# Performance work log

Hardware: AMD Instinct MI355X
Metric: run time of the kernel (lower is better)

Reference implementation:

```python
import jax, jax.numpy as jnp
import numpy as np

B, T, C = 8, 1024, 2048
N_HEAD = 16
HEAD = C // N_HEAD  # 128


def setup_inputs() -> dict:
    key = jax.random.key(0)
    k1, k2, k3 = jax.random.split(key, 3)
    scale = 0.02
    x = jax.random.normal(k1, (B, T, C), dtype=jnp.float32)
    W_attn = jax.random.normal(k2, (C, 3 * C), dtype=jnp.float32) * scale
    b_attn = jnp.zeros((3 * C,), dtype=jnp.float32)
    W_proj = jax.random.normal(k3, (C, C), dtype=jnp.float32) * scale
    b_proj = jnp.zeros((C,), dtype=jnp.float32)
    return {"x": x, "W_attn": W_attn, "b_attn": b_attn, "W_proj": W_proj, "b_proj": b_proj}


def reference(x, W_attn, b_attn, W_proj, b_proj):
    Bq, Tq, Cq = x.shape
    qkv = x @ W_attn + b_attn                       # [B,T,3C]
    q, k, v = jnp.split(qkv, 3, axis=2)             # each [B,T,C]
    def heads(t):
        return t.reshape(Bq, Tq, N_HEAD, HEAD).transpose(0, 2, 1, 3)  # [B,H,T,D]
    q, k, v = heads(q), heads(k), heads(v)
    scores = jnp.einsum('bhqd,bhkd->bhqk', q, k) / jnp.sqrt(jnp.float32(HEAD))
    causal = jnp.tril(jnp.ones((Tq, Tq), dtype=bool))
    scores = jnp.where(causal, scores, jnp.float32(-1e9))
    attn = jax.nn.softmax(scores, axis=-1)          # [B,H,T,T]
    y = jnp.einsum('bhqk,bhkd->bhqd', attn, v)      # [B,H,T,D]
    y = y.transpose(0, 2, 1, 3).reshape(Bq, Tq, Cq) # [B,T,C]
    return y @ W_proj + b_proj
```

## Files before the change

kernel.cpp:

```cpp
#include <hip/hip_runtime.h>
#include <hip/hip_bf16.h>


typedef unsigned short u16;
typedef __bf16 bf16x8 __attribute__((ext_vector_type(8)));
typedef float f32x4 __attribute__((ext_vector_type(4)));

#define B_ 8
#define T_ 1024
#define C_ 2048
#define NH 16
#define HD 128
#define BH (B_*NH)

__device__ __forceinline__ u16 f2b(float f){
  __bf16 h = (__bf16)f; return __builtin_bit_cast(u16, h);
}
__device__ __forceinline__ unsigned pk2(float x, float y){
  return (unsigned)f2b(x) | ((unsigned)f2b(y) << 16);
}
__device__ __forceinline__ bf16x8 ldfrag(const u16* p){
  uint4 u = *(const uint4*)p; return __builtin_bit_cast(bf16x8, u);
}
__device__ __forceinline__ void glds16(const u16* g, const u16* l){
  __builtin_amdgcn_global_load_lds(
      (const __attribute__((address_space(1))) void*)g,
      (__attribute__((address_space(3))) void*)l, 16, 0, 0);
}

__global__ __launch_bounds__(256) void cvt_bf16(
    const float4* __restrict__ in, ushort4* __restrict__ outp, int n4)
{
  int i = blockIdx.x*256 + threadIdx.x;
  const int stride = gridDim.x*256;
  for (; i < n4; i += stride){
    float4 f = in[i];
    ushort4 o; o.x = f2b(f.x); o.y = f2b(f.y); o.z = f2b(f.z); o.w = f2b(f.w);
    outp[i] = o;
  }
}

__global__ __launch_bounds__(256) void transpose_cvt(
    const float* __restrict__ in, u16* __restrict__ outp, int R, int C)
{
  __shared__ u16 tile[64][65];
  const int t = threadIdx.x;
  const int r0 = blockIdx.y * 64, c0 = blockIdx.x * 64;
#pragma unroll
  for (int ii = 0; ii < 16; ++ii){
    int idx = t + ii*256; int r = idx >> 6, c = idx & 63;
    tile[r][c] = f2b(in[(size_t)(r0 + r)*C + c0 + c]);
  }
  __syncthreads();
#pragma unroll
  for (int ii = 0; ii < 16; ++ii){
    int idx = t + ii*256; int r = idx >> 6, c = idx & 63;
    outp[(size_t)(c0 + r)*R + r0 + c] = tile[c][r];
  }
}

__device__ __forceinline__ void qkv_epilogue(
    const f32x4 acc[4][4], const float* bias, int bx, int by,
    int wm, int wn, int lq, int ln,
    u16* qb, u16* kb, u16* vb)
{
  const int tensor = bx >> 4, h = bx & 15, b = by >> 3, t0 = (by & 7)*128;
  u16* tb = tensor==0 ? qb : (tensor==1 ? kb : vb);
  u16* op = tb + ((size_t)(b*NH + h)*T_ + t0)*HD;
#pragma unroll
  for (int j=0;j<4;j++){
    const float bv = bias[bx*128 + wn*64 + j*16 + ln];
    const int n = wn*64 + j*16 + ln;
#pragma unroll
    for (int i=0;i<4;i++){
      const int m0 = wm*64 + i*16 + lq*4;
#pragma unroll
      for (int r=0;r<4;r++)
        op[(size_t)(m0 + r)*HD + n] = f2b(acc[i][j][r] + bv);
    }
  }
}

__global__ __launch_bounds__(256,2) void gemm_qkv_bb(
    const u16* __restrict__ Xb, const u16* __restrict__ Wt, const float* __restrict__ bias,
    u16* __restrict__ qb, u16* __restrict__ kb, u16* __restrict__ vb)
{
  __shared__ u16 As[128*32];
  __shared__ u16 Bs[128*32];
  const int t = threadIdx.x;
  const int bx = blockIdx.x, by = blockIdx.y;
  const int lane = t & 63, wv = t >> 6;
  const int lq = lane >> 4, ln = lane & 15;
  const int wm = wv >> 1, wn = wv & 1;

  const int c0 = t, c1 = 256 + t;
  const u16* Ap0 = Xb + (size_t)(by*128 + (c0 >> 2))*2048 + (c0 & 3)*8;
  const u16* Ap1 = Xb + (size_t)(by*128 + (c1 >> 2))*2048 + (c1 & 3)*8;
  const u16* Bp0 = Wt + (size_t)(bx*128 + (c0 >> 2))*2048 + (c0 & 3)*8;
  const u16* Bp1 = Wt + (size_t)(bx*128 + (c1 >> 2))*2048 + (c1 & 3)*8;
  const u16* AsW0 = &As[(wv*64)*8];
  const u16* AsW1 = &As[(256 + wv*64)*8];
  const u16* BsW0 = &Bs[(wv*64)*8];
  const u16* BsW1 = &Bs[(256 + wv*64)*8];

  const f32x4 fz = {0.f,0.f,0.f,0.f};
  f32x4 acc[4][4];
#pragma unroll
  for (int i=0;i<4;i++)
#pragma unroll
    for (int j=0;j<4;j++) acc[i][j] = fz;

  for (int kt = 0; kt < 64; ++kt){
    __syncthreads();
    glds16(Ap0, AsW0); glds16(Ap1, AsW1);
    glds16(Bp0, BsW0); glds16(Bp1, BsW1);
    Ap0 += 32; Ap1 += 32; Bp0 += 32; Bp1 += 32;
    __syncthreads();
    bf16x8 af[4], bf[4];
#pragma unroll
    for (int i=0;i<4;i++) af[i] = ldfrag(&As[(wm*64 + i*16 + ln)*32 + lq*8]);
#pragma unroll
    for (int j=0;j<4;j++) bf[j] = ldfrag(&Bs[(wn*64 + j*16 + ln)*32 + lq*8]);
#pragma unroll
    for (int i=0;i<4;i++)
#pragma unroll
      for (int j=0;j<4;j++)
        acc[i][j] = __builtin_amdgcn_mfma_f32_16x16x32_bf16(af[i], bf[j], acc[i][j], 0,0,0);
  }
  qkv_epilogue(acc, bias, bx, by, wm, wn, lq, ln, qb, kb, vb);
}

__global__ __launch_bounds__(256,2) void gemm_qkv_f32(
    const float* __restrict__ X, const u16* __restrict__ Wt, const float* __restrict__ bias,
    u16* __restrict__ qb, u16* __restrict__ kb, u16* __restrict__ vb)
{
  __shared__ u16 As[128*32];
  __shared__ u16 Bs[128*32];
  const int t = threadIdx.x;
  const int bx = blockIdx.x, by = blockIdx.y;
  const int lane = t & 63, wv = t >> 6;
  const int lq = lane >> 4, ln = lane & 15;
  const int wm = wv >> 1, wn = wv & 1;

  const int ar = t >> 1, ah = t & 1;
  const float* Ap = X + (size_t)(by*128 + ar)*2048 + ah*16;
  u16* AsW = &As[ar*32 + ah*16];

  const int c0 = t, c1 = 256 + t;
  const u16* Bp0 = Wt + (size_t)(bx*128 + (c0 >> 2))*2048 + (c0 & 3)*8;
  const u16* Bp1 = Wt + (size_t)(bx*128 + (c1 >> 2))*2048 + (c1 & 3)*8;
  const u16* BsW0 = &Bs[(wv*64)*8];
  const u16* BsW1 = &Bs[(256 + wv*64)*8];

  const f32x4 fz = {0.f,0.f,0.f,0.f};
  f32x4 acc[4][4];
#pragma unroll
  for (int i=0;i<4;i++)
#pragma unroll
    for (int j=0;j<4;j++) acc[i][j] = fz;

  for (int kt = 0; kt < 64; ++kt){
    float4 a0 = *(const float4*)(Ap);
    float4 a1 = *(const float4*)(Ap + 4);
    float4 a2 = *(const float4*)(Ap + 8);
    float4 a3 = *(const float4*)(Ap + 12);
    Ap += 32;
    __syncthreads();
    uint4 w0, w1;
    w0.x = pk2(a0.x,a0.y); w0.y = pk2(a0.z,a0.w);
    w0.z = pk2(a1.x,a1.y); w0.w = pk2(a1.z,a1.w);
    w1.x = pk2(a2.x,a2.y); w1.y = pk2(a2.z,a2.w);
    w1.z = pk2(a3.x,a3.y); w1.w = pk2(a3.z,a3.w);
    *(uint4*)(AsW) = w0; *(uint4*)(AsW + 8) = w1;
    glds16(Bp0, BsW0);
    glds16(Bp1, BsW1);
    Bp0 += 32; Bp1 += 32;
    __syncthreads();
    bf16x8 af[4], bf[4];
#pragma unroll
    for (int i=0;i<4;i++) af[i] = ldfrag(&As[(wm*64 + i*16 + ln)*32 + lq*8]);
#pragma unroll
    for (int j=0;j<4;j++) bf[j] = ldfrag(&Bs[(wn*64 + j*16 + ln)*32 + lq*8]);
#pragma unroll
    for (int i=0;i<4;i++)
#pragma unroll
      for (int j=0;j<4;j++)
        acc[i][j] = __builtin_amdgcn_mfma_f32_16x16x32_bf16(af[i], bf[j], acc[i][j], 0,0,0);
  }
  qkv_epilogue(acc, bias, bx, by, wm, wn, lq, ln, qb, kb, vb);
}

__global__ __launch_bounds__(256,2) void gemm_proj(
    const u16* __restrict__ Y, const u16* __restrict__ Wt, const float* __restrict__ bias,
    float* __restrict__ outp)
{
  __shared__ u16 As[128*32];
  __shared__ u16 Bs[128*32];
  const int t = threadIdx.x;
  const int bx = blockIdx.x, by = blockIdx.y;
  const int lane = t & 63, wv = t >> 6;
  const int lq = lane >> 4, ln = lane & 15;
  const int wm = wv >> 1, wn = wv & 1;

  const int c0 = t, c1 = 256 + t;
  const int rA0 = by*128 + (c0 >> 2), rA1 = by*128 + (c1 >> 2);
  const u16* Ya0 = Y + ((size_t)((rA0 >> 10)*NH)*T_ + (rA0 & 1023))*HD;
  const u16* Ya1 = Y + ((size_t)((rA1 >> 10)*NH)*T_ + (rA1 & 1023))*HD;
  const int kc0 = (c0 & 3)*8, kc1 = (c1 & 3)*8;
  const u16* AsW0 = &As[(wv*64)*8];
  const u16* AsW1 = &As[(256 + wv*64)*8];

  const u16* Bp0 = Wt + (size_t)(bx*128 + (c0 >> 2))*2048 + (c0 & 3)*8;
  const u16* Bp1 = Wt + (size_t)(bx*128 + (c1 >> 2))*2048 + (c1 & 3)*8;
  const u16* BsW0 = &Bs[(wv*64)*8];
  const u16* BsW1 = &Bs[(256 + wv*64)*8];

  const f32x4 fz = {0.f,0.f,0.f,0.f};
  f32x4 acc[4][4];
#pragma unroll
  for (int i=0;i<4;i++)
#pragma unroll
    for (int j=0;j<4;j++) acc[i][j] = fz;

  for (int kt = 0; kt < 64; ++kt){
    __syncthreads();
    {
      const int k0 = kt*32 + kc0, k1 = kt*32 + kc1;
      glds16(Ya0 + (size_t)(k0 >> 7)*(T_*HD) + (k0 & 127), AsW0);
      glds16(Ya1 + (size_t)(k1 >> 7)*(T_*HD) + (k1 & 127), AsW1);
      glds16(Bp0, BsW0);
      glds16(Bp1, BsW1);
      Bp0 += 32; Bp1 += 32;
    }
    __syncthreads();
    bf16x8 af[4], bf[4];
#pragma unroll
    for (int i=0;i<4;i++) af[i] = ldfrag(&As[(wm*64 + i*16 + ln)*32 + lq*8]);
#pragma unroll
    for (int j=0;j<4;j++) bf[j] = ldfrag(&Bs[(wn*64 + j*16 + ln)*32 + lq*8]);
#pragma unroll
    for (int i=0;i<4;i++)
#pragma unroll
      for (int j=0;j<4;j++)
        acc[i][j] = __builtin_amdgcn_mfma_f32_16x16x32_bf16(af[i], bf[j], acc[i][j], 0,0,0);
  }

  float* op = outp + (size_t)(by*128)*2048 + bx*128;
#pragma unroll
  for (int j=0;j<4;j++){
    const float bv = bias[bx*128 + wn*64 + j*16 + ln];
    const int n = wn*64 + j*16 + ln;
#pragma unroll
    for (int i=0;i<4;i++){
      const int m0 = wm*64 + i*16 + lq*4;
#pragma unroll
      for (int r=0;r<4;r++)
        op[(size_t)(m0 + r)*2048 + n] = acc[i][j][r] + bv;
    }
  }
}

__global__ __launch_bounds__(256,2) void attn_fwd(
    u16* qy, const u16* __restrict__ kk, const u16* __restrict__ vv)
{
  __shared__ u16 Ks[64*128];
  __shared__ u16 Vt[128*64];
  __shared__ u16 Ps[4*32*64];
  const int qt = 7 - blockIdx.x, bh = blockIdx.y;
  const int t = threadIdx.x;
  const int lane = t & 63, wv = t >> 6;
  const int lq = lane >> 4, ln = lane & 15;

  bf16x8 qf[2][4];
#pragma unroll
  for (int i=0;i<2;i++)
#pragma unroll
    for (int kc=0;kc<4;kc++){
      int qrow = qt*128 + wv*32 + i*16 + ln;
      qf[i][kc] = ldfrag(&qy[((size_t)bh*T_ + qrow)*HD + kc*32 + lq*8]);
    }

  const f32x4 fz = {0.f,0.f,0.f,0.f};
  f32x4 o[2][8];
#pragma unroll
  for (int i=0;i<2;i++)
#pragma unroll
    for (int jd=0;jd<8;jd++) o[i][jd] = fz;
  float mi[2][4], li[2][4];
#pragma unroll
  for (int i=0;i<2;i++)
#pragma unroll
    for (int r=0;r<4;r++){ mi[i][r] = -1e30f; li[i][r] = 0.f; }

  const float scale = 0.08838834764831843f;
  const int kr = t & 63, dbase = (t >> 6)*32;
  const int nkt = 2*qt + 2;
  for (int kt = 0; kt < nkt; ++kt){
    uint4 kreg[4];
    uint4 vreg[4];
    const uint4* ksrc = (const uint4*)(kk + ((size_t)bh*T_ + kt*64)*HD);
#pragma unroll
    for (int ii=0; ii<4; ++ii) kreg[ii] = ksrc[t + ii*256];
#pragma unroll
    for (int ch=0; ch<4; ++ch)
      vreg[ch] = *(const uint4*)&vv[((size_t)bh*T_ + kt*64 + kr)*HD + dbase + ch*8];
    __syncthreads();
    uint4* kdst = (uint4*)Ks;
#pragma unroll
    for (int ii=0; ii<4; ++ii){
      const int c = t + ii*256;
      kdst[(c & ~15) | ((c & 15) ^ ((c >> 4) & 7))] = kreg[ii];
    }
#pragma unroll
    for (int ch=0; ch<4; ++ch){
      const u16* e = (const u16*)&vreg[ch];
#pragma unroll
      for (int j=0; j<8; ++j){
        const int d = dbase + ch*8 + j;
        Vt[d*64 + (kr ^ ((d & 7) << 3))] = e[j];
      }
    }
    __syncthreads();

    f32x4 s[2][4];
#pragma unroll
    for (int i=0;i<2;i++)
#pragma unroll
      for (int j=0;j<4;j++) s[i][j] = fz;
#pragma unroll
    for (int j=0;j<4;j++){
      bf16x8 kf[4];
      const int krow = j*16 + ln;
      const int ksw = (krow & 7) << 3;
#pragma unroll
      for (int kc=0;kc<4;kc++)
        kf[kc] = ldfrag(&Ks[krow*128 + ((kc*32 + lq*8) ^ ksw)]);
#pragma unroll
      for (int i=0;i<2;i++)
#pragma unroll
        for (int kc=0;kc<4;kc++)
          s[i][j] = __builtin_amdgcn_mfma_f32_16x16x32_bf16(qf[i][kc], kf[kc], s[i][j], 0,0,0);
    }

#pragma unroll
    for (int i=0;i<2;i++)
#pragma unroll
      for (int j=0;j<4;j++)
#pragma unroll
        for (int r=0;r<4;r++){
          int qg = qt*128 + wv*32 + i*16 + lq*4 + r;
          int kg = kt*64 + j*16 + ln;
          float sv = s[i][j][r]*scale;
          s[i][j][r] = (kg > qg) ? -1e30f : sv;
        }

#pragma unroll
    for (int i=0;i<2;i++)
#pragma unroll
      for (int r=0;r<4;r++){
        float mx = fmaxf(fmaxf(s[i][0][r], s[i][1][r]), fmaxf(s[i][2][r], s[i][3][r]));
        mx = fmaxf(mx, __shfl_xor(mx, 1));
        mx = fmaxf(mx, __shfl_xor(mx, 2));
        mx = fmaxf(mx, __shfl_xor(mx, 4));
        mx = fmaxf(mx, __shfl_xor(mx, 8));
        float mnew = fmaxf(mi[i][r], mx);
        float alpha = __expf(mi[i][r] - mnew);
        float rs = 0.f;
#pragma unroll
        for (int j=0;j<4;j++){
          float p = __expf(s[i][j][r] - mnew);
          s[i][j][r] = p; rs += p;
        }
        rs += __shfl_xor(rs, 1); rs += __shfl_xor(rs, 2);
        rs += __shfl_xor(rs, 4); rs += __shfl_xor(rs, 8);
        li[i][r] = li[i][r]*alpha + rs;
        mi[i][r] = mnew;
#pragma unroll
        for (int jd=0;jd<8;jd++) o[i][jd][r] *= alpha;
      }

#pragma unroll
    for (int i=0;i<2;i++)
#pragma unroll
      for (int j=0;j<4;j++)
#pragma unroll
        for (int r=0;r<4;r++){
          const int rr = i*16 + lq*4 + r;
          Ps[wv*2048 + rr*64 + ((j*16 + ln) ^ ((rr & 7) << 3))] = f2b(s[i][j][r]);
        }

    bf16x8 pf[2][2];
#pragma unroll
    for (int i=0;i<2;i++){
      const int prow = i*16 + ln;
      const int psw = (prow & 7) << 3;
#pragma unroll
      for (int kc=0;kc<2;kc++)
        pf[i][kc] = ldfrag(&Ps[wv*2048 + prow*64 + ((kc*32 + lq*8) ^ psw)]);
    }
#pragma unroll
    for (int jd=0;jd<8;jd++){
      const int vrow = jd*16 + ln;
      const int vsw = (vrow & 7) << 3;
#pragma unroll
      for (int kc=0;kc<2;kc++){
        bf16x8 vf = ldfrag(&Vt[vrow*64 + ((kc*32 + lq*8) ^ vsw)]);
#pragma unroll
        for (int i=0;i<2;i++)
          o[i][jd] = __builtin_amdgcn_mfma_f32_16x16x32_bf16(pf[i][kc], vf, o[i][jd], 0,0,0);
      }
    }
  }

#pragma unroll
  for (int i=0;i<2;i++)
#pragma unroll
    for (int r=0;r<4;r++){
      float inv = 1.f / li[i][r];
      int row = qt*128 + wv*32 + i*16 + lq*4 + r;
#pragma unroll
      for (int jd=0;jd<8;jd++)
        qy[((size_t)bh*T_ + row)*HD + jd*16 + ln] = f2b(o[i][jd][r] * inv);
    }
}

extern "C" void kernel_launch(void* const* d_in, const int* in_sizes, int n_in,
                              void* d_out, int out_size, void* d_ws, size_t ws_size,
                              hipStream_t stream)
{
  const float* x      = (const float*)d_in[0];
  const float* W_attn = (const float*)d_in[1];
  const float* b_attn = (const float*)d_in[2];
  const float* W_proj = (const float*)d_in[3];
  const float* b_proj = (const float*)d_in[4];
  float* out = (float*)d_out;

  u16* Wat = (u16*)d_ws;
  u16* Wpt = Wat + (size_t)6144*2048;
  u16* qb  = Wpt + (size_t)2048*2048;
  u16* xb  = qb  + (size_t)BH*T_*HD;
  u16* kb  = (u16*)d_out;
  u16* vb  = kb + (size_t)BH*T_*HD;

  const size_t need = ((size_t)6144*2048 + (size_t)2048*2048
                       + 2*(size_t)BH*T_*HD) * sizeof(u16);

  hipLaunchKernelGGL(transpose_cvt, dim3(96,32,1), dim3(256,1,1), 0, stream,
                     W_attn, Wat, 2048, 6144);
  hipLaunchKernelGGL(transpose_cvt, dim3(32,32,1), dim3(256,1,1), 0, stream,
                     W_proj, Wpt, 2048, 2048);
  if (ws_size >= need){
    hipLaunchKernelGGL(cvt_bf16, dim3(1024,1,1), dim3(256,1,1), 0, stream,
                       (const float4*)x, (ushort4*)xb, (B_*T_*C_)/4);
    hipLaunchKernelGGL(gemm_qkv_bb, dim3(48,64,1), dim3(256,1,1), 0, stream,
                       xb, Wat, b_attn, qb, kb, vb);
  } else {
    hipLaunchKernelGGL(gemm_qkv_f32, dim3(48,64,1), dim3(256,1,1), 0, stream,
                       x, Wat, b_attn, qb, kb, vb);
  }
  hipLaunchKernelGGL(attn_fwd, dim3(8,BH,1), dim3(256,1,1), 0, stream,
                     qb, kb, vb);
  hipLaunchKernelGGL(gemm_proj, dim3(16,64,1), dim3(256,1,1), 0, stream,
                     qb, Wpt, b_proj, out);
}
```

Before: 643.3 us.

## Prefetch next K/V tile into registers, add setprio and lazy softmax rescale

The attention loop now loads the next K/V tile into registers right after the shared-memory stores, so global loads overlap the current tile's MFMA and softmax work. MFMA blocks are wrapped in s_setprio to favour matrix issue across waves. Softmax rescaling of the output accumulators is skipped unless some row's max grows by more than a threshold, decided wave-uniformly. This trades extra live registers and larger unnormalised probabilities for less load latency and fewer per-tile multiplies.

```diff
diff --git a/kernel.cpp b/kernel.cpp
--- a/kernel.cpp
+++ b/kernel.cpp
@@ -295,15 +295,19 @@
   const float scale = 0.08838834764831843f;
   const int kr = t & 63, dbase = (t >> 6)*32;
   const int nkt = 2*qt + 2;
+
+  uint4 kreg[4];
+  uint4 vreg[4];
+  {
+    const uint4* ksrc = (const uint4*)(kk + (size_t)bh*T_*HD);
+#pragma unroll
+    for (int ii=0; ii<4; ++ii) kreg[ii] = ksrc[t + ii*256];
+#pragma unroll
+    for (int ch=0; ch<4; ++ch)
+      vreg[ch] = *(const uint4*)&vv[((size_t)bh*T_ + kr)*HD + dbase + ch*8];
+  }
+
   for (int kt = 0; kt < nkt; ++kt){
-    uint4 kreg[4];
-    uint4 vreg[4];
-    const uint4* ksrc = (const uint4*)(kk + ((size_t)bh*T_ + kt*64)*HD);
-#pragma unroll
-    for (int ii=0; ii<4; ++ii) kreg[ii] = ksrc[t + ii*256];
-#pragma unroll
-    for (int ch=0; ch<4; ++ch)
-      vreg[ch] = *(const uint4*)&vv[((size_t)bh*T_ + kt*64 + kr)*HD + dbase + ch*8];
     __syncthreads();
     uint4* kdst = (uint4*)Ks;
 #pragma unroll
@@ -322,11 +326,22 @@
     }
     __syncthreads();
 
+    {
+      const int ktn = (kt+1 < nkt) ? kt+1 : kt;
+      const uint4* ksrc = (const uint4*)(kk + ((size_t)bh*T_ + ktn*64)*HD);
+#pragma unroll
+      for (int ii=0; ii<4; ++ii) kreg[ii] = ksrc[t + ii*256];
+#pragma unroll
+      for (int ch=0; ch<4; ++ch)
+        vreg[ch] = *(const uint4*)&vv[((size_t)bh*T_ + ktn*64 + kr)*HD + dbase + ch*8];
+    }
+
     f32x4 s[2][4];
 #pragma unroll
     for (int i=0;i<2;i++)
 #pragma unroll
       for (int j=0;j<4;j++) s[i][j] = fz;
+    __builtin_amdgcn_s_setprio(1);
 #pragma unroll
     for (int j=0;j<4;j++){
       bf16x8 kf[4];
@@ -341,6 +356,7 @@
         for (int kc=0;kc<4;kc++)
           s[i][j] = __builtin_amdgcn_mfma_f32_16x16x32_bf16(qf[i][kc], kf[kc], s[i][j], 0,0,0);
     }
+    __builtin_amdgcn_s_setprio(0);
 
 #pragma unroll
     for (int i=0;i<2;i++)
@@ -354,6 +370,7 @@
           s[i][j][r] = (kg > qg) ? -1e30f : sv;
         }
 
+    float mxv[2][4];
 #pragma unroll
     for (int i=0;i<2;i++)
 #pragma unroll
@@ -363,20 +380,39 @@
         mx = fmaxf(mx, __shfl_xor(mx, 2));
         mx = fmaxf(mx, __shfl_xor(mx, 4));
         mx = fmaxf(mx, __shfl_xor(mx, 8));
-        float mnew = fmaxf(mi[i][r], mx);
-        float alpha = __expf(mi[i][r] - mnew);
+        mxv[i][r] = mx;
+      }
+    bool ok = true;
+#pragma unroll
+    for (int i=0;i<2;i++)
+#pragma unroll
+      for (int r=0;r<4;r++) ok = ok && (mxv[i][r] <= mi[i][r] + 8.0f);
+    if (!__all((int)ok)){
+#pragma unroll
+      for (int i=0;i<2;i++)
+#pragma unroll
+        for (int r=0;r<4;r++){
+          float mnew = fmaxf(mi[i][r], mxv[i][r]);
+          float alpha = __expf(mi[i][r] - mnew);
+          li[i][r] *= alpha;
+          mi[i][r] = mnew;
+#pragma unroll
+          for (int jd=0;jd<8;jd++) o[i][jd][r] *= alpha;
+        }
+    }
+#pragma unroll
+    for (int i=0;i<2;i++)
+#pragma unroll
+      for (int r=0;r<4;r++){
         float rs = 0.f;
 #pragma unroll
         for (int j=0;j<4;j++){
-          float p = __expf(s[i][j][r] - mnew);
+          float p = __expf(s[i][j][r] - mi[i][r]);
           s[i][j][r] = p; rs += p;
         }
         rs += __shfl_xor(rs, 1); rs += __shfl_xor(rs, 2);
         rs += __shfl_xor(rs, 4); rs += __shfl_xor(rs, 8);
-        li[i][r] = li[i][r]*alpha + rs;
-        mi[i][r] = mnew;
-#pragma unroll
-        for (int jd=0;jd<8;jd++) o[i][jd][r] *= alpha;
+        li[i][r] += rs;
       }
 
 #pragma unroll
@@ -398,6 +434,7 @@
       for (int kc=0;kc<2;kc++)
         pf[i][kc] = ldfrag(&Ps[wv*2048 + prow*64 + ((kc*32 + lq*8) ^ psw)]);
     }
+    __builtin_amdgcn_s_setprio(1);
 #pragma unroll
     for (int jd=0;jd<8;jd++){
       const int vrow = jd*16 + ln;
@@ -410,6 +447,7 @@
           o[i][jd] = __builtin_amdgcn_mfma_f32_16x16x32_bf16(pf[i][kc], vf, o[i][jd], 0,0,0);
       }
     }
+    __builtin_amdgcn_s_setprio(0);
   }
 
 #pragma unroll
```

Measured after the change: 647.3 us. Within noise of the previous version (+0.6%).
